# Kernel optimization log

Hardware: AMD Instinct MI355X
Metric: run time of the kernel (lower is better)

Reference implementation:

```python
import jax, jax.numpy as jnp
import numpy as np

N = 50000
E = 1600000
F_IN = 128
MP_UNITS = [32, 32, 32, 32, 16, 16, 16, 16, 8, 8, 8, 8]
MLP_UNITS = [16, 16]
DELTA = 2.0


def _lin(k, fi, fo):
    kw, kb = jax.random.split(k)
    s = 1.0 / np.sqrt(fi)
    W = jax.random.uniform(kw, (fi, fo), minval=-s, maxval=s, dtype=jnp.float32)
    b = jax.random.uniform(kb, (fo,), minval=-s, maxval=s, dtype=jnp.float32)
    return W, b


def setup_inputs() -> dict:
    key = jax.random.key(0)
    ks = jax.random.split(key, 64)
    inp = {}
    inp['x'] = jax.random.normal(ks[0], (N, F_IN), dtype=jnp.float32)
    inp['edge_index'] = jax.random.randint(ks[1], (2, E), 0, N, dtype=jnp.int32)
    inp['edge_weight'] = jax.random.uniform(ks[2], (E,), dtype=jnp.float32)
    inp['Wi'], inp['bi'] = _lin(ks[3], F_IN, F_IN)
    d = F_IN
    for i, u in enumerate(MP_UNITS):
        inp['Wc%d' % i], inp['bc%d' % i] = _lin(ks[4 + i], d, u)
        d = u
    for i, u in enumerate(MLP_UNITS):
        inp['Wm%d' % i], inp['bm%d' % i] = _lin(ks[20 + i], d, u)
        d = u
    inp['Wf'], inp['bf'] = _lin(ks[30], d, 1)
    return inp


def reference(x, edge_index, edge_weight, Wi, bi,
              Wc0, bc0, Wc1, bc1, Wc2, bc2, Wc3, bc3, Wc4, bc4, Wc5, bc5,
              Wc6, bc6, Wc7, bc7, Wc8, bc8, Wc9, bc9, Wc10, bc10, Wc11, bc11,
              Wm0, bm0, Wm1, bm1, Wf, bf):
    n = x.shape[0]
    src, dst = edge_index[0], edge_index[1]
    # delta_gcn_matrix: P = (1-delta) I + delta * D^{-1/2} A D^{-1/2}
    deg = jax.ops.segment_sum(edge_weight, dst, num_segments=n)
    dinv = jnp.where(deg > 0, jax.lax.rsqrt(jnp.maximum(deg, 1e-12)), 0.0)
    w = DELTA * dinv[src] * edge_weight * dinv[dst]  # [E]
    self_w = 1.0 - DELTA

    h = x @ Wi + bi

    def conv(h, W, b):
        hw = h @ W                                        # [N, out]
        msg = hw[src] * w[:, None]                        # gather + scale [E, out]
        agg = jax.ops.segment_sum(msg, dst, num_segments=n)  # scatter-add
        return agg + self_w * hw + b                      # fold in self-loops

    convs = [(Wc0, bc0), (Wc1, bc1), (Wc2, bc2), (Wc3, bc3), (Wc4, bc4), (Wc5, bc5),
             (Wc6, bc6), (Wc7, bc7), (Wc8, bc8), (Wc9, bc9), (Wc10, bc10), (Wc11, bc11)]
    for W, b in convs:
        h = jnp.tanh(conv(h, W, b))
    for W, b in [(Wm0, bm0), (Wm1, bm1)]:
        h = jax.nn.relu(h @ W + b)
    return jnp.tanh(h @ Wf + bf)  # [N, 1]
```

## Files before the change

### kernel.cpp

```cpp
#include <hip/hip_runtime.h>


constexpr int kN = 50000;
constexpr int kE = 1600000;
constexpr float kSelfW = -1.0f;
constexpr int kCAP = 72;
constexpr int PAD_N = 50176;
constexpr int kPROWS = PAD_N / 8;
constexpr int E4  = kE / 4;
constexpr int E4B = (E4 + 255) / 256;
constexpr int NBG = (kN + 255) / 256;

typedef int      v4i __attribute__((ext_vector_type(4)));
typedef float    v4f __attribute__((ext_vector_type(4)));
typedef _Float16 h8v __attribute__((ext_vector_type(8)));

__device__ __forceinline__ int rowmap(int r) {
  return (r & 7) * kPROWS + (r >> 3);
}
__device__ __forceinline__ unsigned packcw(int colMapped, float w) {
  _Float16 h = (_Float16)w;
  unsigned short u;
  __builtin_memcpy(&u, &h, 2);
  return (unsigned)(unsigned short)colMapped | ((unsigned)u << 16);
}
__device__ __forceinline__ float unpw(unsigned e) {
  unsigned short u = (unsigned short)(e >> 16);
  _Float16 h;
  __builtin_memcpy(&h, &u, 2);
  return (float)h;
}
__device__ __forceinline__ unsigned pack2h(float a, float b) {
  _Float16 ha = (_Float16)a, hb = (_Float16)b;
  unsigned short ua, ub;
  __builtin_memcpy(&ua, &ha, 2);
  __builtin_memcpy(&ub, &hb, 2);
  return (unsigned)ua | ((unsigned)ub << 16);
}
__device__ __forceinline__ float fast_tanh(float x) {
  float t = __expf(2.0f * x);
  float r = __builtin_amdgcn_rcpf(t + 1.0f);
  return 1.0f - 2.0f * r;
}

__global__ __launch_bounds__(256)
void prep(int* __restrict__ cnt, const float* __restrict__ Wi,
          const float* __restrict__ bi, const float* __restrict__ Wc0,
          float* __restrict__ Weff, float* __restrict__ beff) {
  if (blockIdx.x < 49) {
    int i = blockIdx.x * 1024 + threadIdx.x * 4;
    *reinterpret_cast<int4*>(cnt + i) = make_int4(0, 0, 0, 0);
  } else {
    int idx = (blockIdx.x - 49) * 256 + threadIdx.x;
    if (idx >= 129 * 32) return;
    int r = idx >> 5, j = idx & 31;
    float acc = 0.0f;
    if (r < 128) {
      for (int k = 0; k < 128; ++k) acc += Wi[r * 128 + k] * Wc0[k * 32 + j];
      Weff[r * 32 + j] = acc;
    } else {
      for (int k = 0; k < 128; ++k) acc += bi[k] * Wc0[k * 32 + j];
      beff[j] = acc;
    }
  }
}

__global__ __launch_bounds__(256)
void cnt_rank_kernel(const int* __restrict__ dst, int* __restrict__ cnt,
                     int* __restrict__ rank, int e4) {
  int i = blockIdx.x * blockDim.x + threadIdx.x;
  if (i >= e4) return;
  int4 d = reinterpret_cast<const int4*>(dst)[i];
  int4 r;
  r.x = atomicAdd(&cnt[rowmap(d.x)], 1);
  r.y = atomicAdd(&cnt[rowmap(d.y)], 1);
  r.z = atomicAdd(&cnt[rowmap(d.z)], 1);
  r.w = atomicAdd(&cnt[rowmap(d.w)], 1);
  reinterpret_cast<int4*>(rank)[i] = r;
}

__global__ __launch_bounds__(256)
void gemm0(const float* __restrict__ X, const float* __restrict__ Weff,
           const float* __restrict__ beff, _Float16* __restrict__ Y, int n) {
  __shared__ float smem[4128];
  for (int idx = threadIdx.x; idx < 128 * 32; idx += 256) {
    int j = idx >> 7, k = idx & 127;
    smem[j * 128 + k] = Weff[k * 32 + j];
  }
  if (threadIdx.x < 32) smem[4096 + threadIdx.x] = beff[threadIdx.x];
  __syncthreads();
  int row = blockIdx.x * 256 + threadIdx.x;
  if (row >= n) return;
  float acc[32];
#pragma unroll
  for (int j = 0; j < 32; ++j) acc[j] = smem[4096 + j];
  const float4* xr = reinterpret_cast<const float4*>(X + (size_t)row * 128);
  const float4* Ws4 = reinterpret_cast<const float4*>(smem);
  for (int k4 = 0; k4 < 32; ++k4) {
    float4 a = xr[k4];
#pragma unroll
    for (int j = 0; j < 32; ++j) {
      float4 wv = Ws4[j * 32 + k4];
      acc[j] += a.x * wv.x + a.y * wv.y + a.z * wv.z + a.w * wv.w;
    }
  }
  h8v* yr = reinterpret_cast<h8v*>(Y + (size_t)rowmap(row) * 32);
#pragma unroll
  for (int j8 = 0; j8 < 4; ++j8) {
    h8v v;
#pragma unroll
    for (int q = 0; q < 8; ++q) v[q] = (_Float16)acc[8 * j8 + q];
    yr[j8] = v;
  }
}

__global__ __launch_bounds__(256)
void build_part(const int* __restrict__ src, const int* __restrict__ dst,
                const float* __restrict__ ew, const int* __restrict__ rank,
                unsigned* __restrict__ ecw, int e4) {
  int p = blockIdx.x & 7;
  int i = (blockIdx.x >> 3) * 256 + threadIdx.x;
  if (i >= e4) return;
  v4i sv = __builtin_nontemporal_load(reinterpret_cast<const v4i*>(src) + i);
  v4i dv = __builtin_nontemporal_load(reinterpret_cast<const v4i*>(dst) + i);
  v4i rv = __builtin_nontemporal_load(reinterpret_cast<const v4i*>(rank) + i);
  v4f wv = __builtin_nontemporal_load(reinterpret_cast<const v4f*>(ew) + i);
#pragma unroll
  for (int c = 0; c < 4; ++c) {
    int d = dv[c];
    if ((d & 7) == p) {
      int r = rv[c];
      if (r < kCAP)
        ecw[(size_t)(p * kPROWS + (d >> 3)) * kCAP + r] =
            packcw(rowmap(sv[c]), wv[c]);
    }
  }
}

__global__ __launch_bounds__(256)
void deg_dinv_wave(const int* __restrict__ cnt, const unsigned* __restrict__ ecw,
                   float* __restrict__ dinv) {
  int lane = threadIdx.x & 63;
  int br = blockIdx.x * 4 + (threadIdx.x >> 6);
  int deg = min(cnt[br], kCAP);
  size_t base = (size_t)br * kCAP;
  float d = 0.0f;
  for (int i = lane; i < deg; i += 64) d += unpw(ecw[base + i]);
#pragma unroll
  for (int off = 32; off > 0; off >>= 1) d += __shfl_xor(d, off, 64);
  if (lane == 0) dinv[br] = (d > 0.0f) ? rsqrtf(fmaxf(d, 1e-12f)) : 0.0f;
}

__global__ __launch_bounds__(256)
void wscale_wave(const int* __restrict__ cnt, unsigned* __restrict__ ecw,
                 const float* __restrict__ dinv) {
  int lane = threadIdx.x & 63;
  int br = blockIdx.x * 4 + (threadIdx.x >> 6);
  int deg = min(cnt[br], kCAP);
  size_t base = (size_t)br * kCAP;
  float dr = 2.0f * dinv[br];
  for (int i = lane; i < kCAP; i += 64) {
    if (i < deg) {
      unsigned e = ecw[base + i];
      int cm = e & 0xFFFFu;
      ecw[base + i] = packcw(cm, dr * dinv[cm] * unpw(e));
    } else {
      ecw[base + i] = 0u;
    }
  }
}

template <int DOUT, int DNEXT, bool FINAL>
__global__ __launch_bounds__(256)
void spmm_fused(const _Float16* __restrict__ HW, const int* __restrict__ cnt,
                const unsigned* __restrict__ ecw, const float* __restrict__ b,
                const float* __restrict__ Wn, void* __restrict__ Out,
                const float* __restrict__ Wm0, const float* __restrict__ bm0,
                const float* __restrict__ Wm1, const float* __restrict__ bm1,
                const float* __restrict__ Wf, const float* __restrict__ bf,
                int n) {
  constexpr int R = 64 / DOUT;
  constexpr int W = DOUT;
  constexpr int L = DOUT / 8;
  constexpr int S = 8;
  constexpr int WST = DNEXT + 1;
  constexpr int JPT = (DNEXT > 0) ? (DNEXT / S) : 1;
  __shared__ float smem[(DNEXT > 0) ? DOUT * WST : 448];
  if constexpr (DNEXT > 0) {
    for (int idx = threadIdx.x; idx < DOUT * DNEXT; idx += 256) {
      int k = idx / DNEXT, j = idx - k * DNEXT;
      smem[k * WST + j] = Wn[idx];
    }
    __syncthreads();
  }
  if constexpr (FINAL) {
    int t = threadIdx.x;
    if (t < 128) smem[t] = Wm0[t];
    if (t < 256) smem[128 + t] = Wm1[t];
    if (t < 16) {
      smem[384 + t] = bm0[t];
      smem[400 + t] = bm1[t];
      smem[416 + t] = Wf[t];
    }
    if (t == 0) smem[432] = bf[0];
    __syncthreads();
  }
  int lane = threadIdx.x & 63;
  int wid = threadIdx.x >> 6;
  int g = lane / W;
  int gl = lane - g * W;
  int ch8 = gl & (L - 1);
  int sub = gl / L;
  int p = blockIdx.x & 7;
  int q = blockIdx.x >> 3;
  int brLocal = q * (4 * R) + wid * R + g;
  int br = p * kPROWS + brLocal;
  int deg = min(cnt[br], kCAP);
  const uint4* ecw4 = reinterpret_cast<const uint4*>(ecw + (size_t)br * kCAP);
  const h8v* HW8 = reinterpret_cast<const h8v*>(HW);
  uint4 ea = ecw4[sub];
  uint4 eb = ecw4[8 + sub];
  h8v a0 = HW8[(size_t)(ea.x & 0xFFFFu) * L + ch8];
  h8v a1 = HW8[(size_t)(ea.y & 0xFFFFu) * L + ch8];
  h8v a2 = HW8[(size_t)(ea.z & 0xFFFFu) * L + ch8];
  h8v a3 = HW8[(size_t)(ea.w & 0xFFFFu) * L + ch8];
  h8v b0 = HW8[(size_t)(eb.x & 0xFFFFu) * L + ch8];
  h8v b1 = HW8[(size_t)(eb.y & 0xFFFFu) * L + ch8];
  h8v b2 = HW8[(size_t)(eb.z & 0xFFFFu) * L + ch8];
  h8v b3 = HW8[(size_t)(eb.w & 0xFFFFu) * L + ch8];
  float wa0 = unpw(ea.x), wa1 = unpw(ea.y), wa2 = unpw(ea.z), wa3 = unpw(ea.w);
  float wb0 = unpw(eb.x), wb1 = unpw(eb.y), wb2 = unpw(eb.z), wb3 = unpw(eb.w);
  float acc[8];
#pragma unroll
  for (int q8 = 0; q8 < 8; ++q8)
    acc[q8] = wa0 * (float)a0[q8] + wa1 * (float)a1[q8] +
              wa2 * (float)a2[q8] + wa3 * (float)a3[q8] +
              wb0 * (float)b0[q8] + wb1 * (float)b1[q8] +
              wb2 * (float)b2[q8] + wb3 * (float)b3[q8];
  if (deg > 64) {
    if (sub < 2) {
      uint4 et = ecw4[16 + sub];
      h8v t0 = HW8[(size_t)(et.x & 0xFFFFu) * L + ch8];
      h8v t1 = HW8[(size_t)(et.y & 0xFFFFu) * L + ch8];
      h8v t2 = HW8[(size_t)(et.z & 0xFFFFu) * L + ch8];
      h8v t3 = HW8[(size_t)(et.w & 0xFFFFu) * L + ch8];
      float u0 = unpw(et.x), u1 = unpw(et.y), u2 = unpw(et.z), u3 = unpw(et.w);
#pragma unroll
      for (int q8 = 0; q8 < 8; ++q8)
        acc[q8] += u0 * (float)t0[q8] + u1 * (float)t1[q8] +
                   u2 * (float)t2[q8] + u3 * (float)t3[q8];
    }
  }
#pragma unroll
  for (int off = W / 2; off >= L; off >>= 1) {
#pragma unroll
    for (int q8 = 0; q8 < 8; ++q8) acc[q8] += __shfl_xor(acc[q8], off, 64);
  }
  int krow = 8 * ch8;
  h8v hsv = HW8[(size_t)br * L + ch8];
  float h[8];
#pragma unroll
  for (int q8 = 0; q8 < 8; ++q8)
    h[q8] = fast_tanh(acc[q8] + kSelfW * (float)hsv[q8] + b[krow + q8]);
  if constexpr (FINAL) {
    int row = (brLocal << 3) | p;
    if (gl == 0 && row < n) {
      float y0[16];
#pragma unroll
      for (int j = 0; j < 16; ++j) {
        float v = smem[384 + j];
#pragma unroll
        for (int k = 0; k < 8; ++k) v += h[k] * smem[k * 16 + j];
        y0[j] = fmaxf(v, 0.0f);
      }
      float y1[16];
#pragma unroll
      for (int j = 0; j < 16; ++j) {
        float v = smem[400 + j];
#pragma unroll
        for (int k = 0; k < 16; ++k) v += y0[k] * smem[128 + k * 16 + j];
        y1[j] = fmaxf(v, 0.0f);
      }
      float z = smem[432];
#pragma unroll
      for (int k = 0; k < 16; ++k) z += y1[k] * smem[416 + k];
      reinterpret_cast<float*>(Out)[row] = fast_tanh(z);
    }
  } else {
    float pj[JPT];
    int jbase = sub * JPT;
#pragma unroll
    for (int jj = 0; jj < JPT; ++jj) {
      int j = jbase + jj;
      float v = 0.0f;
#pragma unroll
      for (int q8 = 0; q8 < 8; ++q8) v += h[q8] * smem[(krow + q8) * WST + j];
      pj[jj] = v;
    }
#pragma unroll
    for (int off = 1; off < L; off <<= 1) {
#pragma unroll
      for (int jj = 0; jj < JPT; ++jj) pj[jj] += __shfl_xor(pj[jj], off, 64);
    }
    if (ch8 == 0) {
      _Float16* op = reinterpret_cast<_Float16*>(Out) + (size_t)br * DNEXT + jbase;
      if constexpr (JPT == 4) {
        uint2 u = make_uint2(pack2h(pj[0], pj[1]), pack2h(pj[2], pj[3]));
        *reinterpret_cast<uint2*>(op) = u;
      } else if constexpr (JPT == 2) {
        *reinterpret_cast<unsigned*>(op) = pack2h(pj[0], pj[1]);
      } else {
        op[0] = (_Float16)pj[0];
      }
    }
  }
}

extern "C" void kernel_launch(void* const* d_in, const int* in_sizes, int n_in,
                              void* d_out, int out_size, void* d_ws, size_t ws_size,
                              hipStream_t stream) {
  const float* x   = (const float*)d_in[0];
  const int*  eidx = (const int*)d_in[1];
  const float* ew  = (const float*)d_in[2];
  const float* Wi  = (const float*)d_in[3];
  const float* bi  = (const float*)d_in[4];
  const float* Wc[12]; const float* bc[12];
  for (int i = 0; i < 12; ++i) {
    Wc[i] = (const float*)d_in[5 + 2 * i];
    bc[i] = (const float*)d_in[6 + 2 * i];
  }
  const float* Wm0 = (const float*)d_in[29]; const float* bm0 = (const float*)d_in[30];
  const float* Wm1 = (const float*)d_in[31]; const float* bm1 = (const float*)d_in[32];
  const float* Wf  = (const float*)d_in[33]; const float* bf  = (const float*)d_in[34];
  float* out = (float*)d_out;

  const int* src = eidx;
  const int* dst = eidx + kE;

  float* wsf = (float*)d_ws;
  size_t off = 0;
  float*     dinv = wsf + off;              off += PAD_N;
  float*     Weff = wsf + off;              off += 128 * 32;
  float*     beff = wsf + off;              off += 64;
  int*       cnt  = (int*)(wsf + off);      off += PAD_N;
  unsigned*  ecw  = (unsigned*)(wsf + off); off += (size_t)PAD_N * kCAP;
  int*       rank = (int*)(wsf + off);      off += kE;
  _Float16*  B16  = (_Float16*)(wsf + off); off += (size_t)PAD_N * 16;
  _Float16*  C16  = (_Float16*)(wsf + off); off += (size_t)PAD_N * 16;

  const int dgb  = PAD_N / 4;
  const int sb32 = PAD_N / 8;
  const int sb16 = PAD_N / 16;
  const int sb8  = PAD_N / 32;

  prep<<<66, 256, 0, stream>>>(cnt, Wi, bi, Wc[0], Weff, beff);
  cnt_rank_kernel<<<E4B, 256, 0, stream>>>(dst, cnt, rank, E4);
  gemm0<<<NBG, 256, 0, stream>>>(x, Weff, beff, B16, kN);
  build_part<<<E4B * 8, 256, 0, stream>>>(src, dst, ew, rank, ecw, E4);
  deg_dinv_wave<<<dgb, 256, 0, stream>>>(cnt, ecw, dinv);
  wscale_wave<<<dgb, 256, 0, stream>>>(cnt, ecw, dinv);

  spmm_fused<32, 32, false><<<sb32, 256, 0, stream>>>(B16, cnt, ecw, bc[0], Wc[1], C16, nullptr, nullptr, nullptr, nullptr, nullptr, nullptr, kN);
  spmm_fused<32, 32, false><<<sb32, 256, 0, stream>>>(C16, cnt, ecw, bc[1], Wc[2], B16, nullptr, nullptr, nullptr, nullptr, nullptr, nullptr, kN);
  spmm_fused<32, 32, false><<<sb32, 256, 0, stream>>>(B16, cnt, ecw, bc[2], Wc[3], C16, nullptr, nullptr, nullptr, nullptr, nullptr, nullptr, kN);
  spmm_fused<32, 16, false><<<sb32, 256, 0, stream>>>(C16, cnt, ecw, bc[3], Wc[4], B16, nullptr, nullptr, nullptr, nullptr, nullptr, nullptr, kN);
  spmm_fused<16, 16, false><<<sb16, 256, 0, stream>>>(B16, cnt, ecw, bc[4], Wc[5], C16, nullptr, nullptr, nullptr, nullptr, nullptr, nullptr, kN);
  spmm_fused<16, 16, false><<<sb16, 256, 0, stream>>>(C16, cnt, ecw, bc[5], Wc[6], B16, nullptr, nullptr, nullptr, nullptr, nullptr, nullptr, kN);
  spmm_fused<16, 16, false><<<sb16, 256, 0, stream>>>(B16, cnt, ecw, bc[6], Wc[7], C16, nullptr, nullptr, nullptr, nullptr, nullptr, nullptr, kN);
  spmm_fused<16, 8, false><<<sb16, 256, 0, stream>>>(C16, cnt, ecw, bc[7], Wc[8], B16, nullptr, nullptr, nullptr, nullptr, nullptr, nullptr, kN);
  spmm_fused<8, 8, false><<<sb8, 256, 0, stream>>>(B16, cnt, ecw, bc[8], Wc[9], C16, nullptr, nullptr, nullptr, nullptr, nullptr, nullptr, kN);
  spmm_fused<8, 8, false><<<sb8, 256, 0, stream>>>(C16, cnt, ecw, bc[9], Wc[10], B16, nullptr, nullptr, nullptr, nullptr, nullptr, nullptr, kN);
  spmm_fused<8, 8, false><<<sb8, 256, 0, stream>>>(B16, cnt, ecw, bc[10], Wc[11], C16, nullptr, nullptr, nullptr, nullptr, nullptr, nullptr, kN);
  spmm_fused<8, 0, true><<<sb8, 256, 0, stream>>>(C16, cnt, ecw, bc[11], nullptr, out, Wm0, bm0, Wm1, bm1, Wf, bf, kN);
}
```

Measured before the change: 524.4 us.

## Fuse count/rank into CSR build and co-launch gemm0 in one kernel

Removes the separate count/rank pass by doing the atomic slot allocation directly inside the partitioned bucket-build kernel, which drops the rank array and its round trip through global memory. The first dense GEMM now runs as extra blocks of the same launch, so it overlaps with the edge build and two kernel launches go away. As a trade-off, slot order within a row is now nondeterministic, and the atomics sit in the 8-way partitioned pass, which could change atomic contention.

```diff
diff --git a/kernel.cpp b/kernel.cpp
--- a/kernel.cpp
+++ b/kernel.cpp
@@ -10,6 +10,7 @@
 constexpr int E4  = kE / 4;
 constexpr int E4B = (E4 + 255) / 256;
 constexpr int NBG = (kN + 255) / 256;
+constexpr int BCG = E4B * 8;
 
 typedef int      v4i __attribute__((ext_vector_type(4)));
 typedef float    v4f __attribute__((ext_vector_type(4)));
@@ -66,73 +67,60 @@
 }
 
 __global__ __launch_bounds__(256)
-void cnt_rank_kernel(const int* __restrict__ dst, int* __restrict__ cnt,
-                     int* __restrict__ rank, int e4) {
-  int i = blockIdx.x * blockDim.x + threadIdx.x;
-  if (i >= e4) return;
-  int4 d = reinterpret_cast<const int4*>(dst)[i];
-  int4 r;
-  r.x = atomicAdd(&cnt[rowmap(d.x)], 1);
-  r.y = atomicAdd(&cnt[rowmap(d.y)], 1);
-  r.z = atomicAdd(&cnt[rowmap(d.z)], 1);
-  r.w = atomicAdd(&cnt[rowmap(d.w)], 1);
-  reinterpret_cast<int4*>(rank)[i] = r;
-}
-
-__global__ __launch_bounds__(256)
-void gemm0(const float* __restrict__ X, const float* __restrict__ Weff,
-           const float* __restrict__ beff, _Float16* __restrict__ Y, int n) {
+void build_cnt_gemm0(const int* __restrict__ src, const int* __restrict__ dst,
+                     const float* __restrict__ ew, int* __restrict__ cnt,
+                     unsigned* __restrict__ ecw,
+                     const float* __restrict__ X,
+                     const float* __restrict__ Weff,
+                     const float* __restrict__ beff,
+                     _Float16* __restrict__ Y, int e4, int n) {
   __shared__ float smem[4128];
-  for (int idx = threadIdx.x; idx < 128 * 32; idx += 256) {
-    int j = idx >> 7, k = idx & 127;
-    smem[j * 128 + k] = Weff[k * 32 + j];
-  }
-  if (threadIdx.x < 32) smem[4096 + threadIdx.x] = beff[threadIdx.x];
-  __syncthreads();
-  int row = blockIdx.x * 256 + threadIdx.x;
-  if (row >= n) return;
-  float acc[32];
-#pragma unroll
-  for (int j = 0; j < 32; ++j) acc[j] = smem[4096 + j];
-  const float4* xr = reinterpret_cast<const float4*>(X + (size_t)row * 128);
-  const float4* Ws4 = reinterpret_cast<const float4*>(smem);
-  for (int k4 = 0; k4 < 32; ++k4) {
-    float4 a = xr[k4];
-#pragma unroll
-    for (int j = 0; j < 32; ++j) {
-      float4 wv = Ws4[j * 32 + k4];
-      acc[j] += a.x * wv.x + a.y * wv.y + a.z * wv.z + a.w * wv.w;
-    }
-  }
-  h8v* yr = reinterpret_cast<h8v*>(Y + (size_t)rowmap(row) * 32);
-#pragma unroll
-  for (int j8 = 0; j8 < 4; ++j8) {
-    h8v v;
-#pragma unroll
-    for (int q = 0; q < 8; ++q) v[q] = (_Float16)acc[8 * j8 + q];
-    yr[j8] = v;
-  }
-}
-
-__global__ __launch_bounds__(256)
-void build_part(const int* __restrict__ src, const int* __restrict__ dst,
-                const float* __restrict__ ew, const int* __restrict__ rank,
-                unsigned* __restrict__ ecw, int e4) {
+  if (blockIdx.x >= BCG) {
+    for (int idx = threadIdx.x; idx < 128 * 32; idx += 256) {
+      int j = idx >> 7, k = idx & 127;
+      smem[j * 128 + k] = Weff[k * 32 + j];
+    }
+    if (threadIdx.x < 32) smem[4096 + threadIdx.x] = beff[threadIdx.x];
+    __syncthreads();
+    int row = (blockIdx.x - BCG) * 256 + threadIdx.x;
+    if (row >= n) return;
+    float acc[32];
+#pragma unroll
+    for (int j = 0; j < 32; ++j) acc[j] = smem[4096 + j];
+    const float4* xr = reinterpret_cast<const float4*>(X + (size_t)row * 128);
+    const float4* Ws4 = reinterpret_cast<const float4*>(smem);
+    for (int k4 = 0; k4 < 32; ++k4) {
+      float4 a = xr[k4];
+#pragma unroll
+      for (int j = 0; j < 32; ++j) {
+        float4 wv = Ws4[j * 32 + k4];
+        acc[j] += a.x * wv.x + a.y * wv.y + a.z * wv.z + a.w * wv.w;
+      }
+    }
+    h8v* yr = reinterpret_cast<h8v*>(Y + (size_t)rowmap(row) * 32);
+#pragma unroll
+    for (int j8 = 0; j8 < 4; ++j8) {
+      h8v v;
+#pragma unroll
+      for (int q = 0; q < 8; ++q) v[q] = (_Float16)acc[8 * j8 + q];
+      yr[j8] = v;
+    }
+    return;
+  }
   int p = blockIdx.x & 7;
   int i = (blockIdx.x >> 3) * 256 + threadIdx.x;
   if (i >= e4) return;
   v4i sv = __builtin_nontemporal_load(reinterpret_cast<const v4i*>(src) + i);
   v4i dv = __builtin_nontemporal_load(reinterpret_cast<const v4i*>(dst) + i);
-  v4i rv = __builtin_nontemporal_load(reinterpret_cast<const v4i*>(rank) + i);
   v4f wv = __builtin_nontemporal_load(reinterpret_cast<const v4f*>(ew) + i);
 #pragma unroll
   for (int c = 0; c < 4; ++c) {
     int d = dv[c];
     if ((d & 7) == p) {
-      int r = rv[c];
+      int br = p * kPROWS + (d >> 3);
+      int r = atomicAdd(&cnt[br], 1);
       if (r < kCAP)
-        ecw[(size_t)(p * kPROWS + (d >> 3)) * kCAP + r] =
-            packcw(rowmap(sv[c]), wv[c]);
+        ecw[(size_t)br * kCAP + r] = packcw(rowmap(sv[c]), wv[c]);
     }
   }
 }
@@ -344,7 +332,6 @@
   float*     beff = wsf + off;              off += 64;
   int*       cnt  = (int*)(wsf + off);      off += PAD_N;
   unsigned*  ecw  = (unsigned*)(wsf + off); off += (size_t)PAD_N * kCAP;
-  int*       rank = (int*)(wsf + off);      off += kE;
   _Float16*  B16  = (_Float16*)(wsf + off); off += (size_t)PAD_N * 16;
   _Float16*  C16  = (_Float16*)(wsf + off); off += (size_t)PAD_N * 16;
 
@@ -354,9 +341,8 @@
   const int sb8  = PAD_N / 32;
 
   prep<<<66, 256, 0, stream>>>(cnt, Wi, bi, Wc[0], Weff, beff);
-  cnt_rank_kernel<<<E4B, 256, 0, stream>>>(dst, cnt, rank, E4);
-  gemm0<<<NBG, 256, 0, stream>>>(x, Weff, beff, B16, kN);
-  build_part<<<E4B * 8, 256, 0, stream>>>(src, dst, ew, rank, ecw, E4);
+  build_cnt_gemm0<<<BCG + NBG, 256, 0, stream>>>(src, dst, ew, cnt, ecw,
+                                                 x, Weff, beff, B16, E4, kN);
   deg_dinv_wave<<<dgb, 256, 0, stream>>>(cnt, ecw, dinv);
   wscale_wave<<<dgb, 256, 0, stream>>>(cnt, ecw, dinv);
 
```

Measured after the change: 481.7 us. 8.1% less time.
